# Kernel tuning notes

Hardware: AMD Instinct MI355X
Metric: run time of the kernel (lower is better)

The kernel has to match this reference:

```python
import jax, jax.numpy as jnp
import numpy as np

IN_CH, C_M, C_N = 512, 512, 128
B, H, W = 16, 56, 56


def setup_inputs() -> dict:
    key = jax.random.key(0)
    ks = jax.random.split(key, 7)
    s = 1.0 / np.sqrt(IN_CH)
    return {
        "x": jax.random.normal(ks[0], (B, IN_CH, H, W), dtype=jnp.float32),
        "wA": jax.random.uniform(ks[1], (C_M, IN_CH), jnp.float32, -s, s),
        "bA": jax.random.uniform(ks[2], (C_M,), jnp.float32, -s, s),
        "wB": jax.random.uniform(ks[3], (C_N, IN_CH), jnp.float32, -s, s),
        "bB": jax.random.uniform(ks[4], (C_N,), jnp.float32, -s, s),
        "wV": jax.random.uniform(ks[5], (C_N, IN_CH), jnp.float32, -s, s),
        "bV": jax.random.uniform(ks[6], (C_N,), jnp.float32, -s, s),
        "K": 1,
    }


def reference(x, wA, bA, wB, bB, wV, bV, K):
    b, c, h, w = x.shape
    c_m, c_n = wA.shape[0], wB.shape[0]
    batch = b // K
    hw = h * w
    N = K * hw
    # 1x1 convs == channel-wise matmuls
    A = jnp.einsum('bchw,mc->bmhw', x, wA) + bA[None, :, None, None]
    Bf = jnp.einsum('bchw,nc->bnhw', x, wB) + bB[None, :, None, None]
    Vf = jnp.einsum('bchw,nc->bnhw', x, wV) + bV[None, :, None, None]
    # (batch, c_m, K*h*w)
    tmpA = A.reshape(batch, K, c_m, hw).transpose(0, 2, 1, 3).reshape(batch, c_m, N)
    # softmax over the spatial dim N (torch Softmax() on 2D -> dim=1)
    tmpB = Bf.reshape(batch, K, c_n, hw).transpose(0, 2, 1, 3).reshape(batch, c_n, N)
    attB = jax.nn.softmax(tmpB, axis=-1).transpose(0, 2, 1)  # (batch, N, c_n)
    # softmax over channel dim c_n
    tmpV = Vf.reshape(batch, K, c_n, hw).transpose(0, 1, 3, 2).reshape(batch, N, c_n)
    attV = jax.nn.softmax(tmpV, axis=-1).transpose(0, 2, 1)  # (batch, c_n, N)
    G = jnp.matmul(tmpA, attB)   # (batch, c_m, c_n) global descriptors
    Z = jnp.matmul(G, attV)      # (batch, c_m, N) distribute
    Z = Z.reshape(batch, c_m, K, hw).transpose(0, 2, 1, 3).reshape(b, c_m, h, w)
    return Z
```

## Files before the change

kernel.cpp:

```cpp
#include <hip/hip_runtime.h>
#include <hip/hip_bf16.h>

#define BATCH 16
#define CIN   512
#define HW    3136
#define CM    512
#define CN    128
#define CBV   256

typedef short short8 __attribute__((ext_vector_type(8)));
typedef float f32x4  __attribute__((ext_vector_type(4)));

#define MFMA(a,b,c) __builtin_amdgcn_mfma_f32_16x16x32_bf16((a),(b),(c),0,0,0)

__device__ __forceinline__ void cvt_store8(__bf16* dst, const float* src) {
  const f32x4 a = *(const f32x4*)src;
  const f32x4 b = *(const f32x4*)(src + 4);
  __attribute__((aligned(16))) __bf16 t[8];
  t[0] = (__bf16)a[0]; t[1] = (__bf16)a[1]; t[2] = (__bf16)a[2]; t[3] = (__bf16)a[3];
  t[4] = (__bf16)b[0]; t[5] = (__bf16)b[1]; t[6] = (__bf16)b[2]; t[7] = (__bf16)b[3];
  *(uint4*)dst = *(uint4*)t;
}

__global__ __launch_bounds__(256) void conv_bv_kernel(
    const float* __restrict__ x,
    const float* __restrict__ wB, const float* __restrict__ bB,
    const float* __restrict__ wV, const float* __restrict__ bV,
    __bf16* __restrict__ BV)
{
  const int s0  = blockIdx.x * 64;
  const int b   = blockIdx.y;
  const int tid = threadIdx.x;
  const int lane = tid & 63;
  const int w    = tid >> 6;
  const int l15  = lane & 15;
  const int q    = lane >> 4;

  __shared__ __attribute__((aligned(16))) __bf16 Wt[256*72];
  __shared__ __attribute__((aligned(16))) __bf16 Xt[64*72];

  f32x4 acc[4][4] = {};

  const float* xb = x + (size_t)b * CIN * HW;
  const int colg = tid & 7, row0 = tid >> 3;
  const int s_l = tid & 63, cb = tid >> 6;

  for (int k0 = 0; k0 < CIN; k0 += 64) {
    #pragma unroll
    for (int p = 0; p < 8; ++p) {
      int row = row0 + 32*p;
      const float* src = (row < 128) ? (wB + row*512) : (wV + (row-128)*512);
      cvt_store8(&Wt[row*72 + colg*8], src + k0 + colg*8);
    }
    #pragma unroll
    for (int p = 0; p < 2; ++p) {
      int cg = cb + 4*p;
      __attribute__((aligned(16))) __bf16 tmp[8];
      #pragma unroll
      for (int j = 0; j < 8; ++j)
        tmp[j] = (__bf16)xb[(size_t)(k0 + cg*8 + j)*HW + s0 + s_l];
      *(uint4*)&Xt[s_l*72 + cg*8] = *(uint4*)tmp;
    }
    __syncthreads();
    #pragma unroll
    for (int kk = 0; kk < 2; ++kk) {
      short8 a[4], bb[4];
      #pragma unroll
      for (int mi = 0; mi < 4; ++mi)
        a[mi] = *(short8*)&Wt[(w*64 + mi*16 + l15)*72 + kk*32 + q*8];
      #pragma unroll
      for (int si = 0; si < 4; ++si)
        bb[si] = *(short8*)&Xt[(si*16 + l15)*72 + kk*32 + q*8];
      #pragma unroll
      for (int mi = 0; mi < 4; ++mi)
        #pragma unroll
        for (int si = 0; si < 4; ++si)
          acc[mi][si] = MFMA(a[mi], bb[si], acc[mi][si]);
    }
    __syncthreads();
  }

  const size_t outb = (size_t)b * CBV * HW;
  #pragma unroll
  for (int mi = 0; mi < 4; ++mi)
    #pragma unroll
    for (int si = 0; si < 4; ++si) {
      int s = s0 + si*16 + l15;
      #pragma unroll
      for (int r = 0; r < 4; ++r) {
        int nch = w*64 + mi*16 + q*4 + r;
        float bias = (nch < CN) ? bB[nch] : bV[nch-CN];
        BV[outb + (size_t)nch*HW + s] = (__bf16)(acc[mi][si][r] + bias);
      }
    }
}

__global__ __launch_bounds__(256) void softmax_b_kernel(__bf16* __restrict__ BV)
{
  const int n = blockIdx.x, b = blockIdx.y;
  __bf16* row = BV + ((size_t)b*CBV + n)*HW;
  const int tid = threadIdx.x;

  float v[13];
  float mx = -1e30f;
  #pragma unroll
  for (int i = 0; i < 13; ++i) {
    int idx = tid + i*256;
    v[i] = (idx < HW) ? (float)row[idx] : -1e30f;
    mx = fmaxf(mx, v[i]);
  }
  #pragma unroll
  for (int off = 32; off > 0; off >>= 1) mx = fmaxf(mx, __shfl_down(mx, off));
  __shared__ float redm[4], reds[4];
  if ((tid & 63) == 0) redm[tid >> 6] = mx;
  __syncthreads();
  float m = fmaxf(fmaxf(redm[0], redm[1]), fmaxf(redm[2], redm[3]));

  float sum = 0.f;
  #pragma unroll
  for (int i = 0; i < 13; ++i) { v[i] = __expf(v[i] - m); sum += v[i]; }
  #pragma unroll
  for (int off = 32; off > 0; off >>= 1) sum += __shfl_down(sum, off);
  if ((tid & 63) == 0) reds[tid >> 6] = sum;
  __syncthreads();
  float inv = 1.0f / (reds[0] + reds[1] + reds[2] + reds[3]);

  #pragma unroll
  for (int i = 0; i < 13; ++i) {
    int idx = tid + i*256;
    if (idx < HW) row[idx] = (__bf16)(v[i] * inv);
  }
}

__global__ __launch_bounds__(256) void softmax_v_t_kernel(
    const __bf16* __restrict__ BV, __bf16* __restrict__ attVT)
{
  const int s0 = blockIdx.x * 64, b = blockIdx.y;
  const int tid = threadIdx.x;
  const int s_l = tid & 63, jg = tid >> 6;
  const __bf16* vb = BV + ((size_t)b*CBV + CN)*HW + s0 + s_l;

  float v[32];
  float mx = -1e30f;
  #pragma unroll
  for (int i = 0; i < 32; ++i) {
    v[i] = (float)vb[(size_t)(jg*32 + i)*HW];
    mx = fmaxf(mx, v[i]);
  }
  __shared__ float red[4][64];
  red[jg][s_l] = mx;
  __syncthreads();
  float m = fmaxf(fmaxf(red[0][s_l], red[1][s_l]), fmaxf(red[2][s_l], red[3][s_l]));
  float sum = 0.f;
  #pragma unroll
  for (int i = 0; i < 32; ++i) { v[i] = __expf(v[i] - m); sum += v[i]; }
  __syncthreads();
  red[jg][s_l] = sum;
  __syncthreads();
  float inv = 1.0f / (red[0][s_l] + red[1][s_l] + red[2][s_l] + red[3][s_l]);

  __shared__ __attribute__((aligned(16))) __bf16 T[64*136];
  #pragma unroll
  for (int u = 0; u < 4; ++u) {
    __attribute__((aligned(16))) __bf16 tmp[8];
    #pragma unroll
    for (int j = 0; j < 8; ++j) tmp[j] = (__bf16)(v[u*8 + j] * inv);
    *(uint4*)&T[s_l*136 + jg*32 + u*8] = *(uint4*)tmp;
  }
  __syncthreads();
  __bf16* dst = attVT + ((size_t)b*HW + s0)*CN;
  const int g = tid & 15, r0 = tid >> 4;
  #pragma unroll
  for (int p = 0; p < 4; ++p) {
    int row = r0 + 16*p;
    *(uint4*)&dst[row*CN + g*8] = *(uint4*)&T[row*136 + g*8];
  }
}

__global__ __launch_bounds__(256) void h_gemm_kernel(
    const float* __restrict__ x, const __bf16* __restrict__ attB,
    float* __restrict__ H)
{
  const int c0 = blockIdx.x * 128, b = blockIdx.y, kc = blockIdx.z;
  const int tid = threadIdx.x, lane = tid & 63, w = tid >> 6;
  const int l15 = lane & 15, q = lane >> 4;

  __shared__ __attribute__((aligned(16))) __bf16 At[128*72];
  __shared__ __attribute__((aligned(16))) __bf16 Bt[128*72];
  f32x4 acc[8][2] = {};

  const float* xb = x + ((size_t)b*CIN + c0)*HW;
  const __bf16* ab = attB + (size_t)b*CBV*HW;
  const int colg = tid & 7, row0 = tid >> 3;

  for (int ki = 0; ki < 7; ++ki) {
    int k0 = kc*448 + ki*64;
    #pragma unroll
    for (int p = 0; p < 4; ++p) {
      int row = row0 + 32*p;
      cvt_store8(&At[row*72 + colg*8], xb + (size_t)row*HW + k0 + colg*8);
    }
    #pragma unroll
    for (int p = 0; p < 4; ++p) {
      int row = row0 + 32*p;
      *(uint4*)&Bt[row*72 + colg*8] = *(const uint4*)(ab + (size_t)row*HW + k0 + colg*8);
    }
    __syncthreads();
    #pragma unroll
    for (int kk = 0; kk < 2; ++kk) {
      short8 a[8], bb[2];
      #pragma unroll
      for (int mi = 0; mi < 8; ++mi)
        a[mi] = *(short8*)&At[(mi*16 + l15)*72 + kk*32 + q*8];
      #pragma unroll
      for (int ni = 0; ni < 2; ++ni)
        bb[ni] = *(short8*)&Bt[(w*32 + ni*16 + l15)*72 + kk*32 + q*8];
      #pragma unroll
      for (int mi = 0; mi < 8; ++mi)
        #pragma unroll
        for (int ni = 0; ni < 2; ++ni)
          acc[mi][ni] = MFMA(a[mi], bb[ni], acc[mi][ni]);
    }
    __syncthreads();
  }

  float* Hb = H + (size_t)b*CIN*CN;
  #pragma unroll
  for (int mi = 0; mi < 8; ++mi)
    #pragma unroll
    for (int ni = 0; ni < 2; ++ni)
      #pragma unroll
      for (int r = 0; r < 4; ++r) {
        int c = c0 + mi*16 + q*4 + r;
        int n = w*32 + ni*16 + l15;
        atomicAdd(&Hb[c*CN + n], acc[mi][ni][r]);
      }
}

__global__ __launch_bounds__(256) void g_gemm_kernel(
    const float* __restrict__ wA, const float* __restrict__ bA,
    const float* __restrict__ H, __bf16* __restrict__ G)
{
  const int m0 = blockIdx.x * 64, b = blockIdx.y;
  const int tid = threadIdx.x, lane = tid & 63, w = tid >> 6;
  const int l15 = lane & 15, q = lane >> 4;

  __shared__ __attribute__((aligned(16))) __bf16 At[64*72];
  __shared__ __attribute__((aligned(16))) __bf16 Bt[128*72];
  f32x4 acc[4][2] = {};

  const float* Hb = H + (size_t)b*CIN*CN;
  const int colg = tid & 7, row0 = tid >> 3;
  const int nn = tid & 127, gh = tid >> 7;

  for (int k0 = 0; k0 < CIN; k0 += 64) {
    #pragma unroll
    for (int p = 0; p < 2; ++p) {
      int row = row0 + 32*p;
      cvt_store8(&At[row*72 + colg*8], wA + (size_t)(m0+row)*CIN + k0 + colg*8);
    }
    #pragma unroll
    for (int p = 0; p < 4; ++p) {
      int g = gh + 2*p;
      __attribute__((aligned(16))) __bf16 tmp[8];
      #pragma unroll
      for (int j = 0; j < 8; ++j)
        tmp[j] = (__bf16)Hb[(size_t)(k0 + g*8 + j)*CN + nn];
      *(uint4*)&Bt[nn*72 + g*8] = *(uint4*)tmp;
    }
    __syncthreads();
    #pragma unroll
    for (int kk = 0; kk < 2; ++kk) {
      short8 a[4], bb[2];
      #pragma unroll
      for (int mi = 0; mi < 4; ++mi)
        a[mi] = *(short8*)&At[(mi*16 + l15)*72 + kk*32 + q*8];
      #pragma unroll
      for (int ni = 0; ni < 2; ++ni)
        bb[ni] = *(short8*)&Bt[(w*32 + ni*16 + l15)*72 + kk*32 + q*8];
      #pragma unroll
      for (int mi = 0; mi < 4; ++mi)
        #pragma unroll
        for (int ni = 0; ni < 2; ++ni)
          acc[mi][ni] = MFMA(a[mi], bb[ni], acc[mi][ni]);
    }
    __syncthreads();
  }

  #pragma unroll
  for (int mi = 0; mi < 4; ++mi)
    #pragma unroll
    for (int ni = 0; ni < 2; ++ni)
      #pragma unroll
      for (int r = 0; r < 4; ++r) {
        int m = m0 + mi*16 + q*4 + r;
        int n = w*32 + ni*16 + l15;
        G[((size_t)b*CM + m)*CN + n] = (__bf16)(acc[mi][ni][r] + bA[m]);
      }
}

__global__ __launch_bounds__(256) void z_gemm_kernel(
    const __bf16* __restrict__ G, const __bf16* __restrict__ attVT,
    float* __restrict__ out)
{
  const int m0 = blockIdx.x * 128, s0 = blockIdx.y * 64, b = blockIdx.z;
  const int tid = threadIdx.x, lane = tid & 63, w = tid >> 6;
  const int l15 = lane & 15, q = lane >> 4;

  __shared__ __attribute__((aligned(16))) __bf16 At[128*136];
  __shared__ __attribute__((aligned(16))) __bf16 Bt[64*136];

  const __bf16* Gb = G + ((size_t)b*CM + m0)*CN;
  const __bf16* Vb = attVT + ((size_t)b*HW + s0)*CN;
  const int g = tid & 15, r0 = tid >> 4;
  #pragma unroll
  for (int p = 0; p < 8; ++p) {
    int row = r0 + 16*p;
    *(uint4*)&At[row*136 + g*8] = *(const uint4*)(Gb + (size_t)row*CN + g*8);
  }
  #pragma unroll
  for (int p = 0; p < 4; ++p) {
    int row = r0 + 16*p;
    *(uint4*)&Bt[row*136 + g*8] = *(const uint4*)(Vb + (size_t)row*CN + g*8);
  }
  __syncthreads();

  f32x4 acc[8] = {};
  #pragma unroll
  for (int kk = 0; kk < 4; ++kk) {
    short8 bb = *(short8*)&Bt[(w*16 + l15)*136 + kk*32 + q*8];
    #pragma unroll
    for (int mi = 0; mi < 8; ++mi) {
      short8 a = *(short8*)&At[(mi*16 + l15)*136 + kk*32 + q*8];
      acc[mi] = MFMA(a, bb, acc[mi]);
    }
  }

  const int s = s0 + w*16 + l15;
  #pragma unroll
  for (int mi = 0; mi < 8; ++mi)
    #pragma unroll
    for (int r = 0; r < 4; ++r) {
      int m = m0 + mi*16 + q*4 + r;
      out[((size_t)b*CM + m)*HW + s] = acc[mi][r];
    }
}

extern "C" void kernel_launch(void* const* d_in, const int* in_sizes, int n_in,
                              void* d_out, int out_size, void* d_ws, size_t ws_size,
                              hipStream_t stream)
{
  (void)in_sizes; (void)n_in; (void)out_size; (void)ws_size;
  const float* x  = (const float*)d_in[0];
  const float* wA = (const float*)d_in[1];
  const float* bA = (const float*)d_in[2];
  const float* wB = (const float*)d_in[3];
  const float* bB = (const float*)d_in[4];
  const float* wV = (const float*)d_in[5];
  const float* bV = (const float*)d_in[6];
  float* out = (float*)d_out;

  char* ws = (char*)d_ws;
  const size_t szBV    = (size_t)BATCH*CBV*HW*2;
  const size_t szAttVT = (size_t)BATCH*HW*CN*2;
  const size_t szH     = (size_t)BATCH*CIN*CN*4;
  __bf16* BV    = (__bf16*)(ws);
  __bf16* attVT = (__bf16*)(ws + szBV);
  float*  H     = (float*) (ws + szBV + szAttVT);
  __bf16* G     = (__bf16*)(ws + szBV + szAttVT + szH);

  conv_bv_kernel    <<<dim3(49,16),  256, 0, stream>>>(x, wB, bB, wV, bV, BV);
  softmax_b_kernel  <<<dim3(128,16), 256, 0, stream>>>(BV);
  softmax_v_t_kernel<<<dim3(49,16),  256, 0, stream>>>(BV, attVT);
  hipMemsetAsync(H, 0, szH, stream);
  h_gemm_kernel     <<<dim3(4,16,7), 256, 0, stream>>>(x, BV, H);
  g_gemm_kernel     <<<dim3(8,16),   256, 0, stream>>>(wA, bA, H, G);
  z_gemm_kernel     <<<dim3(4,49,16),256, 0, stream>>>(G, attVT, out);
}
```

Baseline: 299.8 us.

## Pre-transpose x to bf16 and pre-cast weights; shrink h_gemm tile

Adds a kernel that transposes x into a channel-contiguous bf16 layout and another that casts all weights to bf16 once per call, so conv_bv loads 16-byte vectors instead of gathering strided fp32 scalars. g_gemm also reads the pre-cast wA. h_gemm uses 64-channel tiles instead of 128, doubling the grid for more parallelism. The cost is an extra full pass over x (read fp32, write bf16) plus more workspace, and the old path is kept as a fallback when workspace is too small.

New measurement: 311.4 us. +3.8%, slower.

```diff
diff --git a/kernel.cpp b/kernel.cpp
--- a/kernel.cpp
+++ b/kernel.cpp
@@ -22,44 +22,74 @@
   *(uint4*)dst = *(uint4*)t;
 }
 
+__global__ __launch_bounds__(256) void wcast_kernel(
+    const float* __restrict__ wB, const float* __restrict__ wV,
+    const float* __restrict__ wA, __bf16* __restrict__ Wbf)
+{
+  size_t i = (size_t)blockIdx.x*2048 + (size_t)threadIdx.x*8;
+  const float* src; size_t off;
+  if (i < 65536)       { src = wB; off = i; }
+  else if (i < 131072) { src = wV; off = i - 65536; }
+  else                 { src = wA; off = i - 131072; }
+  cvt_store8(Wbf + i, src + off);
+}
+
+__global__ __launch_bounds__(256) void transpose_x_kernel(
+    const float* __restrict__ x, __bf16* __restrict__ xT)
+{
+  const int s0 = blockIdx.x * 64;
+  const int c0 = blockIdx.y * 128;
+  const int b  = blockIdx.z;
+  const int tid = threadIdx.x;
+  __shared__ __attribute__((aligned(16))) __bf16 T[64*136];
+
+  const float* xb = x + ((size_t)b*CIN + c0)*HW + s0;
+  const int sg = tid & 15, cr = tid >> 4;
+  #pragma unroll
+  for (int p = 0; p < 8; ++p) {
+    int c = cr + 16*p;
+    f32x4 v = *(const f32x4*)(xb + (size_t)c*HW + sg*4);
+    #pragma unroll
+    for (int j = 0; j < 4; ++j) T[(sg*4 + j)*136 + c] = (__bf16)v[j];
+  }
+  __syncthreads();
+  __bf16* dst = xT + ((size_t)b*HW + s0)*CIN + c0;
+  const int cg = tid & 15, sr = tid >> 4;
+  #pragma unroll
+  for (int p = 0; p < 4; ++p) {
+    int srow = sr + 16*p;
+    *(uint4*)&dst[(size_t)srow*CIN + cg*8] = *(uint4*)&T[srow*136 + cg*8];
+  }
+}
+
 __global__ __launch_bounds__(256) void conv_bv_kernel(
-    const float* __restrict__ x,
-    const float* __restrict__ wB, const float* __restrict__ bB,
-    const float* __restrict__ wV, const float* __restrict__ bV,
+    const __bf16* __restrict__ Wbf, const __bf16* __restrict__ xT,
+    const float* __restrict__ bB, const float* __restrict__ bV,
     __bf16* __restrict__ BV)
 {
   const int s0  = blockIdx.x * 64;
   const int b   = blockIdx.y;
   const int tid = threadIdx.x;
-  const int lane = tid & 63;
-  const int w    = tid >> 6;
-  const int l15  = lane & 15;
-  const int q    = lane >> 4;
+  const int lane = tid & 63, w = tid >> 6;
+  const int l15  = lane & 15, q = lane >> 4;
 
   __shared__ __attribute__((aligned(16))) __bf16 Wt[256*72];
   __shared__ __attribute__((aligned(16))) __bf16 Xt[64*72];
 
   f32x4 acc[4][4] = {};
-
-  const float* xb = x + (size_t)b * CIN * HW;
+  const __bf16* xTb = xT + (size_t)b*HW*CIN;
   const int colg = tid & 7, row0 = tid >> 3;
-  const int s_l = tid & 63, cb = tid >> 6;
 
   for (int k0 = 0; k0 < CIN; k0 += 64) {
     #pragma unroll
     for (int p = 0; p < 8; ++p) {
       int row = row0 + 32*p;
-      const float* src = (row < 128) ? (wB + row*512) : (wV + (row-128)*512);
-      cvt_store8(&Wt[row*72 + colg*8], src + k0 + colg*8);
+      *(uint4*)&Wt[row*72 + colg*8] = *(const uint4*)(Wbf + (size_t)row*CIN + k0 + colg*8);
     }
     #pragma unroll
     for (int p = 0; p < 2; ++p) {
-      int cg = cb + 4*p;
-      __attribute__((aligned(16))) __bf16 tmp[8];
-      #pragma unroll
-      for (int j = 0; j < 8; ++j)
-        tmp[j] = (__bf16)xb[(size_t)(k0 + cg*8 + j)*HW + s0 + s_l];
-      *(uint4*)&Xt[s_l*72 + cg*8] = *(uint4*)tmp;
+      int row = row0 + 32*p;
+      *(uint4*)&Xt[row*72 + colg*8] = *(const uint4*)(xTb + (size_t)(s0+row)*CIN + k0 + colg*8);
     }
     __syncthreads();
     #pragma unroll
@@ -95,6 +125,76 @@
     }
 }
 
+__global__ __launch_bounds__(256) void conv_bv_gather_kernel(
+    const float* __restrict__ x,
+    const float* __restrict__ wB, const float* __restrict__ bB,
+    const float* __restrict__ wV, const float* __restrict__ bV,
+    __bf16* __restrict__ BV)
+{
+  const int s0  = blockIdx.x * 64;
+  const int b   = blockIdx.y;
+  const int tid = threadIdx.x;
+  const int lane = tid & 63, w = tid >> 6;
+  const int l15  = lane & 15, q = lane >> 4;
+
+  __shared__ __attribute__((aligned(16))) __bf16 Wt[256*72];
+  __shared__ __attribute__((aligned(16))) __bf16 Xt[64*72];
+
+  f32x4 acc[4][4] = {};
+  const float* xb = x + (size_t)b * CIN * HW;
+  const int colg = tid & 7, row0 = tid >> 3;
+  const int s_l = tid & 63, cb = tid >> 6;
+
+  for (int k0 = 0; k0 < CIN; k0 += 64) {
+    #pragma unroll
+    for (int p = 0; p < 8; ++p) {
+      int row = row0 + 32*p;
+      const float* src = (row < 128) ? (wB + row*512) : (wV + (row-128)*512);
+      cvt_store8(&Wt[row*72 + colg*8], src + k0 + colg*8);
+    }
+    #pragma unroll
+    for (int p = 0; p < 2; ++p) {
+      int cg = cb + 4*p;
+      __attribute__((aligned(16))) __bf16 tmp[8];
+      #pragma unroll
+      for (int j = 0; j < 8; ++j)
+        tmp[j] = (__bf16)xb[(size_t)(k0 + cg*8 + j)*HW + s0 + s_l];
+      *(uint4*)&Xt[s_l*72 + cg*8] = *(uint4*)tmp;
+    }
+    __syncthreads();
+    #pragma unroll
+    for (int kk = 0; kk < 2; ++kk) {
+      short8 a[4], bb[4];
+      #pragma unroll
+      for (int mi = 0; mi < 4; ++mi)
+        a[mi] = *(short8*)&Wt[(w*64 + mi*16 + l15)*72 + kk*32 + q*8];
+      #pragma unroll
+      for (int si = 0; si < 4; ++si)
+        bb[si] = *(short8*)&Xt[(si*16 + l15)*72 + kk*32 + q*8];
+      #pragma unroll
+      for (int mi = 0; mi < 4; ++mi)
+        #pragma unroll
+        for (int si = 0; si < 4; ++si)
+          acc[mi][si] = MFMA(a[mi], bb[si], acc[mi][si]);
+    }
+    __syncthreads();
+  }
+
+  const size_t outb = (size_t)b * CBV * HW;
+  #pragma unroll
+  for (int mi = 0; mi < 4; ++mi)
+    #pragma unroll
+    for (int si = 0; si < 4; ++si) {
+      int s = s0 + si*16 + l15;
+      #pragma unroll
+      for (int r = 0; r < 4; ++r) {
+        int nch = w*64 + mi*16 + q*4 + r;
+        float bias = (nch < CN) ? bB[nch] : bV[nch-CN];
+        BV[outb + (size_t)nch*HW + s] = (__bf16)(acc[mi][si][r] + bias);
+      }
+    }
+}
+
 __global__ __launch_bounds__(256) void softmax_b_kernel(__bf16* __restrict__ BV)
 {
   const int n = blockIdx.x, b = blockIdx.y;
@@ -181,13 +281,13 @@
     const float* __restrict__ x, const __bf16* __restrict__ attB,
     float* __restrict__ H)
 {
-  const int c0 = blockIdx.x * 128, b = blockIdx.y, kc = blockIdx.z;
+  const int c0 = blockIdx.x * 64, b = blockIdx.y, kc = blockIdx.z;
   const int tid = threadIdx.x, lane = tid & 63, w = tid >> 6;
   const int l15 = lane & 15, q = lane >> 4;
 
-  __shared__ __attribute__((aligned(16))) __bf16 At[128*72];
+  __shared__ __attribute__((aligned(16))) __bf16 At[64*72];
   __shared__ __attribute__((aligned(16))) __bf16 Bt[128*72];
-  f32x4 acc[8][2] = {};
+  f32x4 acc[4][2] = {};
 
   const float* xb = x + ((size_t)b*CIN + c0)*HW;
   const __bf16* ab = attB + (size_t)b*CBV*HW;
@@ -196,27 +296,27 @@
   for (int ki = 0; ki < 7; ++ki) {
     int k0 = kc*448 + ki*64;
     #pragma unroll
+    for (int p = 0; p < 2; ++p) {
+      int row = row0 + 32*p;
+      cvt_store8(&At[row*72 + colg*8], xb + (size_t)row*HW + k0 + colg*8);
+    }
+    #pragma unroll
     for (int p = 0; p < 4; ++p) {
       int row = row0 + 32*p;
-      cvt_store8(&At[row*72 + colg*8], xb + (size_t)row*HW + k0 + colg*8);
-    }
-    #pragma unroll
-    for (int p = 0; p < 4; ++p) {
-      int row = row0 + 32*p;
       *(uint4*)&Bt[row*72 + colg*8] = *(const uint4*)(ab + (size_t)row*HW + k0 + colg*8);
     }
     __syncthreads();
     #pragma unroll
     for (int kk = 0; kk < 2; ++kk) {
-      short8 a[8], bb[2];
-      #pragma unroll
-      for (int mi = 0; mi < 8; ++mi)
+      short8 a[4], bb[2];
+      #pragma unroll
+      for (int mi = 0; mi < 4; ++mi)
         a[mi] = *(short8*)&At[(mi*16 + l15)*72 + kk*32 + q*8];
       #pragma unroll
       for (int ni = 0; ni < 2; ++ni)
         bb[ni] = *(short8*)&Bt[(w*32 + ni*16 + l15)*72 + kk*32 + q*8];
       #pragma unroll
-      for (int mi = 0; mi < 8; ++mi)
+      for (int mi = 0; mi < 4; ++mi)
         #pragma unroll
         for (int ni = 0; ni < 2; ++ni)
           acc[mi][ni] = MFMA(a[mi], bb[ni], acc[mi][ni]);
@@ -226,7 +326,7 @@
 
   float* Hb = H + (size_t)b*CIN*CN;
   #pragma unroll
-  for (int mi = 0; mi < 8; ++mi)
+  for (int mi = 0; mi < 4; ++mi)
     #pragma unroll
     for (int ni = 0; ni < 2; ++ni)
       #pragma unroll
@@ -238,7 +338,7 @@
 }
 
 __global__ __launch_bounds__(256) void g_gemm_kernel(
-    const float* __restrict__ wA, const float* __restrict__ bA,
+    const __bf16* __restrict__ wAbf, const float* __restrict__ bA,
     const float* __restrict__ H, __bf16* __restrict__ G)
 {
   const int m0 = blockIdx.x * 64, b = blockIdx.y;
@@ -257,7 +357,7 @@
     #pragma unroll
     for (int p = 0; p < 2; ++p) {
       int row = row0 + 32*p;
-      cvt_store8(&At[row*72 + colg*8], wA + (size_t)(m0+row)*CIN + k0 + colg*8);
+      *(uint4*)&At[row*72 + colg*8] = *(const uint4*)(wAbf + (size_t)(m0+row)*CIN + k0 + colg*8);
     }
     #pragma unroll
     for (int p = 0; p < 4; ++p) {
@@ -299,6 +399,68 @@
       }
 }
 
+__global__ __launch_bounds__(256) void g_gemm_f32w_kernel(
+    const float* __restrict__ wA, const float* __restrict__ bA,
+    const float* __restrict__ H, __bf16* __restrict__ G)
+{
+  const int m0 = blockIdx.x * 64, b = blockIdx.y;
+  const int tid = threadIdx.x, lane = tid & 63, w = tid >> 6;
+  const int l15 = lane & 15, q = lane >> 4;
+
+  __shared__ __attribute__((aligned(16))) __bf16 At[64*72];
+  __shared__ __attribute__((aligned(16))) __bf16 Bt[128*72];
+  f32x4 acc[4][2] = {};
+
+  const float* Hb = H + (size_t)b*CIN*CN;
+  const int colg = tid & 7, row0 = tid >> 3;
+  const int nn = tid & 127, gh = tid >> 7;
+
+  for (int k0 = 0; k0 < CIN; k0 += 64) {
+    #pragma unroll
+    for (int p = 0; p < 2; ++p) {
+      int row = row0 + 32*p;
+      cvt_store8(&At[row*72 + colg*8], wA + (size_t)(m0+row)*CIN + k0 + colg*8);
+    }
+    #pragma unroll
+    for (int p = 0; p < 4; ++p) {
+      int g = gh + 2*p;
+      __attribute__((aligned(16))) __bf16 tmp[8];
+      #pragma unroll
+      for (int j = 0; j < 8; ++j)
+        tmp[j] = (__bf16)Hb[(size_t)(k0 + g*8 + j)*CN + nn];
+      *(uint4*)&Bt[nn*72 + g*8] = *(uint4*)tmp;
+    }
+    __syncthreads();
+    #pragma unroll
+    for (int kk = 0; kk < 2; ++kk) {
+      short8 a[4], bb[2];
+      #pragma unroll
+      for (int mi = 0; mi < 4; ++mi)
+        a[mi] = *(short8*)&At[(mi*16 + l15)*72 + kk*32 + q*8];
+      #pragma unroll
+      for (int ni = 0; ni < 2; ++ni)
+        bb[ni] = *(short8*)&Bt[(w*32 + ni*16 + l15)*72 + kk*32 + q*8];
+      #pragma unroll
+      for (int mi = 0; mi < 4; ++mi)
+        #pragma unroll
+        for (int ni = 0; ni < 2; ++ni)
+          acc[mi][ni] = MFMA(a[mi], bb[ni], acc[mi][ni]);
+    }
+    __syncthreads();
+  }
+
+  #pragma unroll
+  for (int mi = 0; mi < 4; ++mi)
+    #pragma unroll
+    for (int ni = 0; ni < 2; ++ni)
+      #pragma unroll
+      for (int r = 0; r < 4; ++r) {
+        int m = m0 + mi*16 + q*4 + r;
+        int n = w*32 + ni*16 + l15;
+        G[((size_t)b*CM + m)*CN + n] = (__bf16)(acc[mi][ni][r] + bA[m]);
+      }
+}
+
 __global__ __launch_bounds__(256) void z_gemm_kernel(
     const __bf16* __restrict__ G, const __bf16* __restrict__ attVT,
     float* __restrict__ out)
@@ -350,7 +512,7 @@
                               void* d_out, int out_size, void* d_ws, size_t ws_size,
                               hipStream_t stream)
 {
-  (void)in_sizes; (void)n_in; (void)out_size; (void)ws_size;
+  (void)in_sizes; (void)n_in; (void)out_size;
   const float* x  = (const float*)d_in[0];
   const float* wA = (const float*)d_in[1];
   const float* bA = (const float*)d_in[2];
@@ -361,19 +523,44 @@
   float* out = (float*)d_out;
 
   char* ws = (char*)d_ws;
+  const size_t szXT    = (size_t)BATCH*HW*CIN*2;
+  const size_t szWBF   = (size_t)(128*512 + 128*512 + 512*512)*2;
   const size_t szBV    = (size_t)BATCH*CBV*HW*2;
   const size_t szAttVT = (size_t)BATCH*HW*CN*2;
   const size_t szH     = (size_t)BATCH*CIN*CN*4;
-  __bf16* BV    = (__bf16*)(ws);
-  __bf16* attVT = (__bf16*)(ws + szBV);
-  float*  H     = (float*) (ws + szBV + szAttVT);
-  __bf16* G     = (__bf16*)(ws + szBV + szAttVT + szH);
-
-  conv_bv_kernel    <<<dim3(49,16),  256, 0, stream>>>(x, wB, bB, wV, bV, BV);
-  softmax_b_kernel  <<<dim3(128,16), 256, 0, stream>>>(BV);
-  softmax_v_t_kernel<<<dim3(49,16),  256, 0, stream>>>(BV, attVT);
-  hipMemsetAsync(H, 0, szH, stream);
-  h_gemm_kernel     <<<dim3(4,16,7), 256, 0, stream>>>(x, BV, H);
-  g_gemm_kernel     <<<dim3(8,16),   256, 0, stream>>>(wA, bA, H, G);
-  z_gemm_kernel     <<<dim3(4,49,16),256, 0, stream>>>(G, attVT, out);
-}
+  const size_t szG     = (size_t)BATCH*CM*CN*2;
+  const size_t needMain = szXT + szWBF + szBV + szAttVT + szH + szG;
+
+  if (ws_size >= needMain) {
+    __bf16* xT    = (__bf16*)(ws);
+    __bf16* Wbf   = (__bf16*)(ws + szXT);
+    __bf16* BV    = (__bf16*)(ws + szXT + szWBF);
+    __bf16* attVT = (__bf16*)(ws + szXT + szWBF + szBV);
+    float*  H     = (float*) (ws + szXT + szWBF + szBV + szAttVT);
+    __bf16* G     = (__bf16*)(ws + szXT + szWBF + szBV + szAttVT + szH);
+    __bf16* wAbf  = Wbf + 2*128*512;
+
+    wcast_kernel      <<<dim3(192),     256, 0, stream>>>(wB, wV, wA, Wbf);
+    transpose_x_kernel<<<dim3(49,4,16), 256, 0, stream>>>(x, xT);
+    conv_bv_kernel    <<<dim3(49,16),   256, 0, stream>>>(Wbf, xT, bB, bV, BV);
+    softmax_b_kernel  <<<dim3(128,16),  256, 0, stream>>>(BV);
+    softmax_v_t_kernel<<<dim3(49,16),   256, 0, stream>>>(BV, attVT);
+    hipMemsetAsync(H, 0, szH, stream);
+    h_gemm_kernel     <<<dim3(8,16,7),  256, 0, stream>>>(x, BV, H);
+    g_gemm_kernel     <<<dim3(8,16),    256, 0, stream>>>(wAbf, bA, H, G);
+    z_gemm_kernel     <<<dim3(4,49,16), 256, 0, stream>>>(G, attVT, out);
+  } else {
+    __bf16* BV    = (__bf16*)(ws);
+    __bf16* attVT = (__bf16*)(ws + szBV);
+    float*  H     = (float*) (ws + szBV + szAttVT);
+    __bf16* G     = (__bf16*)(ws + szBV + szAttVT + szH);
+
+    conv_bv_gather_kernel<<<dim3(49,16),   256, 0, stream>>>(x, wB, bB, wV, bV, BV);
+    softmax_b_kernel     <<<dim3(128,16),  256, 0, stream>>>(BV);
+    softmax_v_t_kernel   <<<dim3(49,16),   256, 0, stream>>>(BV, attVT);
+    hipMemsetAsync(H, 0, szH, stream);
+    h_gemm_kernel        <<<dim3(8,16,7),  256, 0, stream>>>(x, BV, H);
+    g_gemm_f32w_kernel   <<<dim3(8,16),    256, 0, stream>>>(wA, bA, H, G);
+    z_gemm_kernel        <<<dim3(4,49,16), 256, 0, stream>>>(G, attVT, out);
+  }
+}
```

## Pre-transpose x to bf16, fuse V softmax into conv, split B softmax stats

Applied to the files above, without the earlier changes.

Adds a weight cast kernel and a kernel that transposes x into a channel-contiguous bf16 layout, so the B/V projection GEMM can load both operands with vectorised reads instead of strided scalar reads with per-element conversion. The channel softmax over V is computed in the conv epilogue from the accumulators and written out transposed, which removes the separate softmax_v kernel. The spatial softmax on B is reduced to a row-stats kernel (max and reciprocal sum), and the exponentials are applied on the fly when h_gemm loads its operand. The cost is an extra pass over x to write xT, a larger workspace, and recomputing exp inside h_gemm.

Result: no change. 305.0 us (+1.7%).

```diff
diff --git a/kernel.cpp b/kernel.cpp
--- a/kernel.cpp
+++ b/kernel.cpp
@@ -22,44 +22,92 @@
   *(uint4*)dst = *(uint4*)t;
 }
 
+__global__ __launch_bounds__(256) void wcast_kernel(
+    const float* __restrict__ wB, const float* __restrict__ wV,
+    const float* __restrict__ wA, __bf16* __restrict__ Wbf)
+{
+  size_t i = (size_t)blockIdx.x*2048 + (size_t)threadIdx.x*8;
+  const float* src; size_t off;
+  if (i < 65536)       { src = wB; off = i; }
+  else if (i < 131072) { src = wV; off = i - 65536; }
+  else                 { src = wA; off = i - 131072; }
+  cvt_store8(Wbf + i, src + off);
+}
+
+__global__ __launch_bounds__(256) void transpose_x_kernel(
+    const float* __restrict__ x, __bf16* __restrict__ xT)
+{
+  const int s0 = blockIdx.x * 64;
+  const int c0 = blockIdx.y * 128;
+  const int b  = blockIdx.z;
+  const int tid = threadIdx.x;
+  __shared__ __attribute__((aligned(16))) __bf16 T[64*136];
+
+  const float* xb = x + ((size_t)b*CIN + c0)*HW + s0;
+  const int colg = tid & 7;
+  const int pr   = tid >> 3;
+
+  #pragma unroll
+  for (int p = 0; p < 2; ++p) {
+    int c = (pr + 32*p) * 2;
+    const float* r0 = xb + (size_t)c*HW + colg*8;
+    const float* r1 = r0 + HW;
+    f32x4 a0 = *(const f32x4*)r0, a1 = *(const f32x4*)(r0 + 4);
+    f32x4 b0 = *(const f32x4*)r1, b1 = *(const f32x4*)(r1 + 4);
+    float va[8] = {a0[0],a0[1],a0[2],a0[3],a1[0],a1[1],a1[2],a1[3]};
+    float vb[8] = {b0[0],b0[1],b0[2],b0[3],b1[0],b1[1],b1[2],b1[3]};
+    const int off = ((c >> 3) ^ colg) * 8 + (c & 7);
+    #pragma unroll
+    for (int j = 0; j < 8; ++j) {
+      int s = colg*8 + j;
+      __attribute__((aligned(4))) __bf16 pairv[2] = { (__bf16)va[j], (__bf16)vb[j] };
+      *(unsigned int*)&T[s*136 + off] = *(unsigned int*)pairv;
+    }
+  }
+  __syncthreads();
+
+  __bf16* dst = xT + ((size_t)b*HW + s0)*CIN + c0;
+  const int cg = tid & 15, sr = tid >> 4;
+  #pragma unroll
+  for (int p = 0; p < 4; ++p) {
+    int row = sr + 16*p;
+    int oct = cg ^ ((row >> 3) & 7);
+    *(uint4*)&dst[(size_t)row*CIN + cg*8] = *(uint4*)&T[row*136 + oct*8];
+  }
+}
+
 __global__ __launch_bounds__(256) void conv_bv_kernel(
-    const float* __restrict__ x,
-    const float* __restrict__ wB, const float* __restrict__ bB,
-    const float* __restrict__ wV, const float* __restrict__ bV,
-    __bf16* __restrict__ BV)
+    const __bf16* __restrict__ Wbf, const __bf16* __restrict__ xT,
+    const float* __restrict__ bB, const float* __restrict__ bV,
+    __bf16* __restrict__ BVB, __bf16* __restrict__ attVT)
 {
   const int s0  = blockIdx.x * 64;
   const int b   = blockIdx.y;
   const int tid = threadIdx.x;
-  const int lane = tid & 63;
-  const int w    = tid >> 6;
-  const int l15  = lane & 15;
-  const int q    = lane >> 4;
-
-  __shared__ __attribute__((aligned(16))) __bf16 Wt[256*72];
-  __shared__ __attribute__((aligned(16))) __bf16 Xt[64*72];
+  const int lane = tid & 63, w = tid >> 6;
+  const int l15  = lane & 15, q = lane >> 4;
+
+  __shared__ __attribute__((aligned(16))) char smem[46080];
+  __bf16* Wt = (__bf16*)smem;
+  __bf16* Xt = (__bf16*)(smem + 36864);
+  __bf16* T  = (__bf16*)smem;
+  __shared__ float Vm[2][64];
+  __shared__ float Vs[2][64];
 
   f32x4 acc[4][4] = {};
-
-  const float* xb = x + (size_t)b * CIN * HW;
+  const __bf16* xTb = xT + (size_t)b*HW*CIN;
   const int colg = tid & 7, row0 = tid >> 3;
-  const int s_l = tid & 63, cb = tid >> 6;
 
   for (int k0 = 0; k0 < CIN; k0 += 64) {
     #pragma unroll
     for (int p = 0; p < 8; ++p) {
       int row = row0 + 32*p;
-      const float* src = (row < 128) ? (wB + row*512) : (wV + (row-128)*512);
-      cvt_store8(&Wt[row*72 + colg*8], src + k0 + colg*8);
+      *(uint4*)&Wt[row*72 + colg*8] = *(const uint4*)(Wbf + (size_t)row*CIN + k0 + colg*8);
     }
     #pragma unroll
     for (int p = 0; p < 2; ++p) {
-      int cg = cb + 4*p;
-      __attribute__((aligned(16))) __bf16 tmp[8];
-      #pragma unroll
-      for (int j = 0; j < 8; ++j)
-        tmp[j] = (__bf16)xb[(size_t)(k0 + cg*8 + j)*HW + s0 + s_l];
-      *(uint4*)&Xt[s_l*72 + cg*8] = *(uint4*)tmp;
+      int row = row0 + 32*p;
+      *(uint4*)&Xt[row*72 + colg*8] = *(const uint4*)(xTb + (size_t)(s0+row)*CIN + k0 + colg*8);
     }
     __syncthreads();
     #pragma unroll
@@ -80,105 +128,133 @@
     __syncthreads();
   }
 
-  const size_t outb = (size_t)b * CBV * HW;
+  float bias[4][4];
   #pragma unroll
   for (int mi = 0; mi < 4; ++mi)
     #pragma unroll
+    for (int r = 0; r < 4; ++r) {
+      int nch = w*64 + mi*16 + q*4 + r;
+      bias[mi][r] = (nch < CN) ? bB[nch] : bV[nch - CN];
+    }
+
+  if (w < 2) {
+    const size_t outb = (size_t)b * CN * HW;
+    #pragma unroll
+    for (int mi = 0; mi < 4; ++mi)
+      #pragma unroll
+      for (int si = 0; si < 4; ++si) {
+        int s = s0 + si*16 + l15;
+        #pragma unroll
+        for (int r = 0; r < 4; ++r) {
+          int nch = w*64 + mi*16 + q*4 + r;
+          BVB[outb + (size_t)nch*HW + s] = (__bf16)(acc[mi][si][r] + bias[mi][r]);
+        }
+      }
+  } else {
+    #pragma unroll
     for (int si = 0; si < 4; ++si) {
-      int s = s0 + si*16 + l15;
-      #pragma unroll
-      for (int r = 0; r < 4; ++r) {
-        int nch = w*64 + mi*16 + q*4 + r;
-        float bias = (nch < CN) ? bB[nch] : bV[nch-CN];
-        BV[outb + (size_t)nch*HW + s] = (__bf16)(acc[mi][si][r] + bias);
-      }
-    }
-}
-
-__global__ __launch_bounds__(256) void softmax_b_kernel(__bf16* __restrict__ BV)
-{
-  const int n = blockIdx.x, b = blockIdx.y;
-  __bf16* row = BV + ((size_t)b*CBV + n)*HW;
-  const int tid = threadIdx.x;
-
-  float v[13];
-  float mx = -1e30f;
-  #pragma unroll
-  for (int i = 0; i < 13; ++i) {
-    int idx = tid + i*256;
-    v[i] = (idx < HW) ? (float)row[idx] : -1e30f;
-    mx = fmaxf(mx, v[i]);
-  }
-  #pragma unroll
-  for (int off = 32; off > 0; off >>= 1) mx = fmaxf(mx, __shfl_down(mx, off));
-  __shared__ float redm[4], reds[4];
-  if ((tid & 63) == 0) redm[tid >> 6] = mx;
+      float m = -1e30f;
+      #pragma unroll
+      for (int mi = 0; mi < 4; ++mi)
+        #pragma unroll
+        for (int r = 0; r < 4; ++r)
+          m = fmaxf(m, acc[mi][si][r] + bias[mi][r]);
+      m = fmaxf(m, __shfl_xor(m, 16));
+      m = fmaxf(m, __shfl_xor(m, 32));
+      if (q == 0) Vm[w-2][si*16 + l15] = m;
+    }
+  }
   __syncthreads();
-  float m = fmaxf(fmaxf(redm[0], redm[1]), fmaxf(redm[2], redm[3]));
-
-  float sum = 0.f;
-  #pragma unroll
-  for (int i = 0; i < 13; ++i) { v[i] = __expf(v[i] - m); sum += v[i]; }
-  #pragma unroll
-  for (int off = 32; off > 0; off >>= 1) sum += __shfl_down(sum, off);
-  if ((tid & 63) == 0) reds[tid >> 6] = sum;
+  if (w >= 2) {
+    #pragma unroll
+    for (int si = 0; si < 4; ++si) {
+      int idx = si*16 + l15;
+      float ms = fmaxf(Vm[0][idx], Vm[1][idx]);
+      float ssum = 0.f;
+      #pragma unroll
+      for (int mi = 0; mi < 4; ++mi)
+        #pragma unroll
+        for (int r = 0; r < 4; ++r) {
+          float e = __expf(acc[mi][si][r] + bias[mi][r] - ms);
+          acc[mi][si][r] = e;
+          ssum += e;
+        }
+      ssum += __shfl_xor(ssum, 16);
+      ssum += __shfl_xor(ssum, 32);
+      if (q == 0) Vs[w-2][idx] = ssum;
+    }
+  }
   __syncthreads();
-  float inv = 1.0f / (reds[0] + reds[1] + reds[2] + reds[3]);
-
-  #pragma unroll
-  for (int i = 0; i < 13; ++i) {
-    int idx = tid + i*256;
-    if (idx < HW) row[idx] = (__bf16)(v[i] * inv);
-  }
-}
-
-__global__ __launch_bounds__(256) void softmax_v_t_kernel(
-    const __bf16* __restrict__ BV, __bf16* __restrict__ attVT)
-{
-  const int s0 = blockIdx.x * 64, b = blockIdx.y;
-  const int tid = threadIdx.x;
-  const int s_l = tid & 63, jg = tid >> 6;
-  const __bf16* vb = BV + ((size_t)b*CBV + CN)*HW + s0 + s_l;
-
-  float v[32];
-  float mx = -1e30f;
-  #pragma unroll
-  for (int i = 0; i < 32; ++i) {
-    v[i] = (float)vb[(size_t)(jg*32 + i)*HW];
-    mx = fmaxf(mx, v[i]);
-  }
-  __shared__ float red[4][64];
-  red[jg][s_l] = mx;
-  __syncthreads();
-  float m = fmaxf(fmaxf(red[0][s_l], red[1][s_l]), fmaxf(red[2][s_l], red[3][s_l]));
-  float sum = 0.f;
-  #pragma unroll
-  for (int i = 0; i < 32; ++i) { v[i] = __expf(v[i] - m); sum += v[i]; }
-  __syncthreads();
-  red[jg][s_l] = sum;
-  __syncthreads();
-  float inv = 1.0f / (red[0][s_l] + red[1][s_l] + red[2][s_l] + red[3][s_l]);
-
-  __shared__ __attribute__((aligned(16))) __bf16 T[64*136];
-  #pragma unroll
-  for (int u = 0; u < 4; ++u) {
-    __attribute__((aligned(16))) __bf16 tmp[8];
-    #pragma unroll
-    for (int j = 0; j < 8; ++j) tmp[j] = (__bf16)(v[u*8 + j] * inv);
-    *(uint4*)&T[s_l*136 + jg*32 + u*8] = *(uint4*)tmp;
+  if (w >= 2) {
+    #pragma unroll
+    for (int si = 0; si < 4; ++si) {
+      int idx = si*16 + l15;
+      float inv = 1.0f / (Vs[0][idx] + Vs[1][idx]);
+      #pragma unroll
+      for (int mi = 0; mi < 4; ++mi)
+        #pragma unroll
+        for (int r = 0; r < 4; ++r) {
+          int j = (w-2)*64 + mi*16 + q*4 + r;
+          T[idx*136 + j] = (__bf16)(acc[mi][si][r] * inv);
+        }
+    }
   }
   __syncthreads();
   __bf16* dst = attVT + ((size_t)b*HW + s0)*CN;
-  const int g = tid & 15, r0 = tid >> 4;
-  #pragma unroll
-  for (int p = 0; p < 4; ++p) {
-    int row = r0 + 16*p;
-    *(uint4*)&dst[row*CN + g*8] = *(uint4*)&T[row*136 + g*8];
-  }
+  #pragma unroll
+  for (int k = 0; k < 4; ++k) {
+    int chunk = tid + 256*k;
+    int row = chunk >> 4, oct = chunk & 15;
+    *(uint4*)&dst[(size_t)row*CN + oct*8] = *(uint4*)&T[row*136 + oct*8];
+  }
+}
+
+__global__ __launch_bounds__(256) void bstats_kernel(
+    const __bf16* __restrict__ BVB, float* __restrict__ sm, float* __restrict__ sinv)
+{
+  const int row = blockIdx.x*4 + (threadIdx.x >> 6);
+  const int lane = threadIdx.x & 63;
+  const __bf16* rp = BVB + (size_t)row*HW;
+
+  uint4 raw[7];
+  float mx = -1e30f;
+  #pragma unroll
+  for (int i = 0; i < 6; ++i) {
+    raw[i] = *(const uint4*)(rp + (lane + 64*i)*8);
+    const __bf16* v = (const __bf16*)&raw[i];
+    #pragma unroll
+    for (int j = 0; j < 8; ++j) mx = fmaxf(mx, (float)v[j]);
+  }
+  if (lane < 8) {
+    raw[6] = *(const uint4*)(rp + (lane + 384)*8);
+    const __bf16* v = (const __bf16*)&raw[6];
+    #pragma unroll
+    for (int j = 0; j < 8; ++j) mx = fmaxf(mx, (float)v[j]);
+  }
+  #pragma unroll
+  for (int off = 1; off < 64; off <<= 1) mx = fmaxf(mx, __shfl_xor(mx, off));
+
+  float sum = 0.f;
+  #pragma unroll
+  for (int i = 0; i < 6; ++i) {
+    const __bf16* v = (const __bf16*)&raw[i];
+    #pragma unroll
+    for (int j = 0; j < 8; ++j) sum += __expf((float)v[j] - mx);
+  }
+  if (lane < 8) {
+    const __bf16* v = (const __bf16*)&raw[6];
+    #pragma unroll
+    for (int j = 0; j < 8; ++j) sum += __expf((float)v[j] - mx);
+  }
+  #pragma unroll
+  for (int off = 1; off < 64; off <<= 1) sum += __shfl_xor(sum, off);
+
+  if (lane == 0) { sm[row] = mx; sinv[row] = 1.0f / sum; }
 }
 
 __global__ __launch_bounds__(256) void h_gemm_kernel(
-    const float* __restrict__ x, const __bf16* __restrict__ attB,
+    const float* __restrict__ x, const __bf16* __restrict__ BVB,
+    const float* __restrict__ sm, const float* __restrict__ sinv,
     float* __restrict__ H)
 {
   const int c0 = blockIdx.x * 128, b = blockIdx.y, kc = blockIdx.z;
@@ -190,7 +266,9 @@
   f32x4 acc[8][2] = {};
 
   const float* xb = x + ((size_t)b*CIN + c0)*HW;
-  const __bf16* ab = attB + (size_t)b*CBV*HW;
+  const __bf16* ab = BVB + (size_t)b*CN*HW;
+  const float* smb = sm + b*CN;
+  const float* sib = sinv + b*CN;
   const int colg = tid & 7, row0 = tid >> 3;
 
   for (int ki = 0; ki < 7; ++ki) {
@@ -203,7 +281,14 @@
     #pragma unroll
     for (int p = 0; p < 4; ++p) {
       int row = row0 + 32*p;
-      *(uint4*)&Bt[row*72 + colg*8] = *(const uint4*)(ab + (size_t)row*HW + k0 + colg*8);
+      uint4 rawv = *(const uint4*)(ab + (size_t)row*HW + k0 + colg*8);
+      const __bf16* v = (const __bf16*)&rawv;
+      float mrow = smb[row], irow = sib[row];
+      __attribute__((aligned(16))) __bf16 t[8];
+      #pragma unroll
+      for (int j = 0; j < 8; ++j)
+        t[j] = (__bf16)(__expf((float)v[j] - mrow) * irow);
+      *(uint4*)&Bt[row*72 + colg*8] = *(uint4*)t;
     }
     __syncthreads();
     #pragma unroll
@@ -238,7 +323,7 @@
 }
 
 __global__ __launch_bounds__(256) void g_gemm_kernel(
-    const float* __restrict__ wA, const float* __restrict__ bA,
+    const __bf16* __restrict__ wAbf, const float* __restrict__ bA,
     const float* __restrict__ H, __bf16* __restrict__ G)
 {
   const int m0 = blockIdx.x * 64, b = blockIdx.y;
@@ -257,7 +342,7 @@
     #pragma unroll
     for (int p = 0; p < 2; ++p) {
       int row = row0 + 32*p;
-      cvt_store8(&At[row*72 + colg*8], wA + (size_t)(m0+row)*CIN + k0 + colg*8);
+      *(uint4*)&At[row*72 + colg*8] = *(const uint4*)(wAbf + (size_t)(m0+row)*CIN + k0 + colg*8);
     }
     #pragma unroll
     for (int p = 0; p < 4; ++p) {
@@ -361,19 +446,29 @@
   float* out = (float*)d_out;
 
   char* ws = (char*)d_ws;
-  const size_t szBV    = (size_t)BATCH*CBV*HW*2;
+  const size_t szXT    = (size_t)BATCH*HW*CIN*2;
+  const size_t szWBF   = (size_t)(128*512 + 128*512 + 512*512)*2;
+  const size_t szBVB   = (size_t)BATCH*CN*HW*2;
   const size_t szAttVT = (size_t)BATCH*HW*CN*2;
   const size_t szH     = (size_t)BATCH*CIN*CN*4;
-  __bf16* BV    = (__bf16*)(ws);
-  __bf16* attVT = (__bf16*)(ws + szBV);
-  float*  H     = (float*) (ws + szBV + szAttVT);
-  __bf16* G     = (__bf16*)(ws + szBV + szAttVT + szH);
-
-  conv_bv_kernel    <<<dim3(49,16),  256, 0, stream>>>(x, wB, bB, wV, bV, BV);
-  softmax_b_kernel  <<<dim3(128,16), 256, 0, stream>>>(BV);
-  softmax_v_t_kernel<<<dim3(49,16),  256, 0, stream>>>(BV, attVT);
+
+  char* p = ws;
+  __bf16* xT    = (__bf16*)p; p += szXT;
+  __bf16* Wbf   = (__bf16*)p; p += szWBF;
+  __bf16* BVB   = (__bf16*)p; p += szBVB;
+  __bf16* attVT = (__bf16*)p; p += szAttVT;
+  float*  H     = (float*)p;  p += szH;
+  __bf16* G     = (__bf16*)p; p += (size_t)BATCH*CM*CN*2;
+  float*  sm    = (float*)p;  p += (size_t)BATCH*CN*4;
+  float*  sinv  = (float*)p;
+  __bf16* wAbf  = Wbf + 2*128*512;
+
+  wcast_kernel      <<<dim3(192),     256, 0, stream>>>(wB, wV, wA, Wbf);
+  transpose_x_kernel<<<dim3(49,4,16), 256, 0, stream>>>(x, xT);
+  conv_bv_kernel    <<<dim3(49,16),   256, 0, stream>>>(Wbf, xT, bB, bV, BVB, attVT);
+  bstats_kernel     <<<dim3(512),     256, 0, stream>>>(BVB, sm, sinv);
   hipMemsetAsync(H, 0, szH, stream);
-  h_gemm_kernel     <<<dim3(4,16,7), 256, 0, stream>>>(x, BV, H);
-  g_gemm_kernel     <<<dim3(8,16),   256, 0, stream>>>(wA, bA, H, G);
-  z_gemm_kernel     <<<dim3(4,49,16),256, 0, stream>>>(G, attVT, out);
-}
+  h_gemm_kernel     <<<dim3(4,16,7),  256, 0, stream>>>(x, BVB, sm, sinv, H);
+  g_gemm_kernel     <<<dim3(8,16),    256, 0, stream>>>(wAbf, bA, H, G);
+  z_gemm_kernel     <<<dim3(4,49,16), 256, 0, stream>>>(G, attVT, out);
+}
```
